# Kernel tuning notes

Measured on AMD Instinct MI355X. Metric: run time of the kernel, lower is better.

The kernel has to match this reference:

```python
import jax, jax.numpy as jnp
import numpy as np

NUM_CLASSES = 10000
FEAT_DIM = 512
BATCH = 4096


def setup_inputs() -> dict:
    key = jax.random.key(0)
    k1, k2, k3 = jax.random.split(key, 3)
    x = jax.random.normal(k1, (BATCH, FEAT_DIM), dtype=jnp.float32)
    labels = jax.random.randint(k2, (BATCH,), 0, NUM_CLASSES, dtype=jnp.int64)
    centers = jax.random.normal(k3, (NUM_CLASSES, FEAT_DIM), dtype=jnp.float32)
    return {"x": x, "labels": labels, "centers": centers}


def reference(x, labels, centers):
    batch_size = x.shape[0]
    num_classes = centers.shape[0]
    # distmat[b, c] = ||x_b||^2 + ||center_c||^2 - 2 <x_b, center_c>   (batch, num_classes)
    x_sq = jnp.sum(x * x, axis=1, keepdims=True)              # (B, 1)
    c_sq = jnp.sum(centers * centers, axis=1)[None, :]        # (1, C)
    distmat = x_sq + c_sq - 2.0 * jnp.einsum('bd,cd->bc', x, centers)
    # one-hot mask of the true class per row (faithful to labels.eq(classes))
    mask = (labels[:, None] == jnp.arange(num_classes)[None, :]).astype(distmat.dtype)
    dist = distmat * mask
    # faithful elementwise clamp BEFORE sum: zeroed entries become 1e-12 each
    loss = jnp.sum(jnp.clip(dist, 1e-12, 1e12)) / batch_size
    return loss
```

## Files before the change

kernel.cpp:

```cpp
#include <hip/hip_runtime.h>

#define BATCH 4096
#define FEAT 512
#define NUM_CLASSES 10000

__global__ __launch_bounds__(256) void center_loss_dist(
    const float* __restrict__ x,
    const int* __restrict__ labels,
    const float* __restrict__ centers,
    float* __restrict__ ws) {
    const int wave = threadIdx.x >> 6;
    const int lane = threadIdx.x & 63;
    const int row  = blockIdx.x * 4 + wave;

    const int lbl = labels[row];
    const float4* __restrict__ xr = (const float4*)(x + (size_t)row * FEAT);
    const float4* __restrict__ cr = (const float4*)(centers + (size_t)lbl * FEAT);

    float4 a0 = xr[lane];
    float4 a1 = xr[lane + 64];
    float4 c0 = cr[lane];
    float4 c1 = cr[lane + 64];

    float d0 = a0.x - c0.x, d1 = a0.y - c0.y, d2 = a0.z - c0.z, d3 = a0.w - c0.w;
    float e0 = a1.x - c1.x, e1 = a1.y - c1.y, e2 = a1.z - c1.z, e3 = a1.w - c1.w;
    float acc = d0 * d0 + d1 * d1 + d2 * d2 + d3 * d3
              + e0 * e0 + e1 * e1 + e2 * e2 + e3 * e3;

#pragma unroll
    for (int off = 32; off > 0; off >>= 1)
        acc += __shfl_down(acc, off, 64);

    if (lane == 0) ws[row] = acc;
}

__global__ __launch_bounds__(1024) void center_loss_reduce(
    const float* __restrict__ ws,
    float* __restrict__ out) {
    const int tid = threadIdx.x;
    const float4 v = ((const float4*)ws)[tid];

    float s = fminf(fmaxf(v.x, 1e-12f), 1e12f)
            + fminf(fmaxf(v.y, 1e-12f), 1e12f)
            + fminf(fmaxf(v.z, 1e-12f), 1e12f)
            + fminf(fmaxf(v.w, 1e-12f), 1e12f);

#pragma unroll
    for (int off = 32; off > 0; off >>= 1)
        s += __shfl_down(s, off, 64);

    __shared__ float warp_sums[16];
    const int wave = tid >> 6;
    const int lane = tid & 63;
    if (lane == 0) warp_sums[wave] = s;
    __syncthreads();

    if (wave == 0) {
        float t = (lane < 16) ? warp_sums[lane] : 0.0f;
#pragma unroll
        for (int off = 8; off > 0; off >>= 1)
            t += __shfl_down(t, off, 64);
        if (lane == 0) {
            out[0] = t * (1.0f / (float)BATCH)
                   + (float)((double)(NUM_CLASSES - 1) * 1e-12);
        }
    }
}

extern "C" void kernel_launch(void* const* d_in, const int* in_sizes, int n_in,
                              void* d_out, int out_size, void* d_ws, size_t ws_size,
                              hipStream_t stream) {
    const float* x       = (const float*)d_in[0];
    const int*   labels  = (const int*)d_in[1];
    const float* centers = (const float*)d_in[2];
    float* out = (float*)d_out;
    float* ws  = (float*)d_ws;

    center_loss_dist<<<BATCH / 4, 256, 0, stream>>>(x, labels, centers, ws);
    center_loss_reduce<<<1, 1024, 0, stream>>>(ws, out);
}
```

Baseline: 73.55 us.

## Fuse distance and reduction kernels with last-block atomic finalization

Merges the per-row distance kernel and the single-block reduction into one kernel. Each 1024-thread block handles 16 rows, clamps them, writes its partial sum, and increments an atomic counter, and the last block to finish sums all partials into the output. This removes one kernel launch and the dependency between launches, but adds a memset launch to reset the counter, atomics, and a serialized tail in the last block.

```diff
diff --git a/kernel.cpp b/kernel.cpp
--- a/kernel.cpp
+++ b/kernel.cpp
@@ -3,15 +3,19 @@
 #define BATCH 4096
 #define FEAT 512
 #define NUM_CLASSES 10000
+#define NBLK 256
+#define NTHR 1024
+#define ROWS_PER_BLK (BATCH / NBLK)
 
-__global__ __launch_bounds__(256) void center_loss_dist(
+__global__ __launch_bounds__(NTHR) void center_loss_fused(
     const float* __restrict__ x,
     const int* __restrict__ labels,
     const float* __restrict__ centers,
-    float* __restrict__ ws) {
+    float* __restrict__ ws,
+    float* __restrict__ out) {
     const int wave = threadIdx.x >> 6;
     const int lane = threadIdx.x & 63;
-    const int row  = blockIdx.x * 4 + wave;
+    const int row  = blockIdx.x * ROWS_PER_BLK + wave;
 
     const int lbl = labels[row];
     const float4* __restrict__ xr = (const float4*)(x + (size_t)row * FEAT);
@@ -31,39 +35,34 @@
     for (int off = 32; off > 0; off >>= 1)
         acc += __shfl_down(acc, off, 64);
 
-    if (lane == 0) ws[row] = acc;
-}
-
-__global__ __launch_bounds__(1024) void center_loss_reduce(
-    const float* __restrict__ ws,
-    float* __restrict__ out) {
-    const int tid = threadIdx.x;
-    const float4 v = ((const float4*)ws)[tid];
-
-    float s = fminf(fmaxf(v.x, 1e-12f), 1e12f)
-            + fminf(fmaxf(v.y, 1e-12f), 1e12f)
-            + fminf(fmaxf(v.z, 1e-12f), 1e12f)
-            + fminf(fmaxf(v.w, 1e-12f), 1e12f);
-
-#pragma unroll
-    for (int off = 32; off > 0; off >>= 1)
-        s += __shfl_down(s, off, 64);
-
-    __shared__ float warp_sums[16];
-    const int wave = tid >> 6;
-    const int lane = tid & 63;
-    if (lane == 0) warp_sums[wave] = s;
+    __shared__ float wsum[ROWS_PER_BLK];
+    __shared__ int amLast;
+    if (lane == 0)
+        wsum[wave] = fminf(fmaxf(acc, 1e-12f), 1e12f);
     __syncthreads();
 
-    if (wave == 0) {
-        float t = (lane < 16) ? warp_sums[lane] : 0.0f;
+    if (threadIdx.x == 0) {
+        float p = 0.0f;
 #pragma unroll
-        for (int off = 8; off > 0; off >>= 1)
+        for (int i = 0; i < ROWS_PER_BLK; ++i) p += wsum[i];
+        atomicExch(&ws[64 + blockIdx.x], p);
+        asm volatile("s_waitcnt vmcnt(0) lgkmcnt(0)" ::: "memory");
+        unsigned old = atomicAdd((unsigned int*)ws, 1u);
+        amLast = (old == (unsigned)(NBLK - 1));
+    }
+    __syncthreads();
+
+    if (amLast && wave == 0) {
+        float t = atomicAdd(&ws[64 + lane],        0.0f)
+                + atomicAdd(&ws[64 + 64 + lane],   0.0f)
+                + atomicAdd(&ws[64 + 128 + lane],  0.0f)
+                + atomicAdd(&ws[64 + 192 + lane],  0.0f);
+#pragma unroll
+        for (int off = 32; off > 0; off >>= 1)
             t += __shfl_down(t, off, 64);
-        if (lane == 0) {
+        if (lane == 0)
             out[0] = t * (1.0f / (float)BATCH)
                    + (float)((double)(NUM_CLASSES - 1) * 1e-12);
-        }
     }
 }
 
@@ -73,9 +72,8 @@
     const float* x       = (const float*)d_in[0];
     const int*   labels  = (const int*)d_in[1];
     const float* centers = (const float*)d_in[2];
-    float* out = (float*)d_out;
-    float* ws  = (float*)d_ws;
 
-    center_loss_dist<<<BATCH / 4, 256, 0, stream>>>(x, labels, centers, ws);
-    center_loss_reduce<<<1, 1024, 0, stream>>>(ws, out);
+    hipMemsetAsync(d_ws, 0, 4, stream);
+    center_loss_fused<<<NBLK, NTHR, 0, stream>>>(x, labels, centers,
+                                                 (float*)d_ws, (float*)d_out);
 }
```

After: 78.14 us. 1.06x slower.
